# Optimization experiments

Hardware: AMD Instinct MI355X
Metric: run time of the kernel (lower is better)

## Reference

```python
import jax, jax.numpy as jnp
import numpy as np

B, T, N_POS, N_ACT, H = 256, 512, 128, 32, 512
D = N_POS + N_ACT


def setup_inputs() -> dict:
    key = jax.random.key(0)
    ks = jax.random.split(key, 10)
    s_ih = 1.0 / np.sqrt(H)  # torch LSTMCell default uniform(-1/sqrt(H), 1/sqrt(H))
    xav_hc = np.sqrt(2.0 / (B + H))  # xavier_normal_ on [B,H] h0/c0
    return {
        "observation": jax.random.normal(ks[0], (B, T, N_POS), dtype=jnp.float32),
        "action": jax.random.normal(ks[1], (B, T, N_ACT), dtype=jnp.float32),
        "W_ih": jax.random.uniform(ks[2], (4 * H, D), jnp.float32, -s_ih, s_ih),
        "W_hh": jax.random.uniform(ks[3], (4 * H, H), jnp.float32, -s_ih, s_ih),
        "b_ih": jax.random.uniform(ks[4], (4 * H,), jnp.float32, -s_ih, s_ih),
        "b_hh": jax.random.uniform(ks[5], (4 * H,), jnp.float32, -s_ih, s_ih),
        "W_out": jax.random.uniform(ks[6], (1, H), jnp.float32, -s_ih, s_ih),
        "b_out": jax.random.uniform(ks[7], (1,), jnp.float32, -s_ih, s_ih),
        "h0": jax.random.normal(ks[8], (B, H), dtype=jnp.float32) * xav_hc,
        "c0": jax.random.normal(ks[9], (B, H), dtype=jnp.float32) * xav_hc,
    }


def reference(observation, action, W_ih, W_hh, b_ih, b_hh, W_out, b_out, h0, c0):
    # x: [B,T,D] -> scan over time [T,B,D]
    x = jnp.concatenate([observation, action], axis=-1)
    xs = jnp.transpose(x, (1, 0, 2))
    b = b_ih + b_hh

    def step(carry, x_t):
        h, c = carry
        gates = x_t @ W_ih.T + h @ W_hh.T + b  # [B, 4H]
        i, f, g, o = jnp.split(gates, 4, axis=-1)
        i = jax.nn.sigmoid(i)
        f = jax.nn.sigmoid(f)
        g = jnp.tanh(g)
        o = jax.nn.sigmoid(o)
        c_new = f * c + i * g
        h_new = o * jnp.tanh(c_new)
        y = h_new @ W_out.T + b_out  # [B, 1]
        return (h_new, c_new), y

    _, ys = jax.lax.scan(step, (h0, c0), xs)  # ys: [T, B, 1]
    return jnp.transpose(ys, (1, 0, 2))  # [B, T, 1]
```

## Files before the change

kernel.cpp:

```cpp
#include <hip/hip_runtime.h>
#include <math.h>


namespace {
constexpr int kT = 512, kH = 512;

typedef _Float16 v8h __attribute__((ext_vector_type(8)));
typedef float v4f __attribute__((ext_vector_type(4)));
typedef unsigned long long ull;
typedef ull v2u __attribute__((ext_vector_type(2)));

__device__ __forceinline__ ull ld64sc(const ull* p, bool sys) {
    return sys ? __hip_atomic_load(p, __ATOMIC_RELAXED, __HIP_MEMORY_SCOPE_SYSTEM)
               : __hip_atomic_load(p, __ATOMIC_RELAXED, __HIP_MEMORY_SCOPE_AGENT);
}
__device__ __forceinline__ unsigned ld32sc(const unsigned* p, bool sys) {
    return sys ? __hip_atomic_load(p, __ATOMIC_RELAXED, __HIP_MEMORY_SCOPE_SYSTEM)
               : __hip_atomic_load(p, __ATOMIC_RELAXED, __HIP_MEMORY_SCOPE_AGENT);
}
__device__ __forceinline__ void st32sc(unsigned* p, unsigned v, bool sys) {
    if (sys) __hip_atomic_store(p, v, __ATOMIC_RELAXED, __HIP_MEMORY_SCOPE_SYSTEM);
    else     __hip_atomic_store(p, v, __ATOMIC_RELAXED, __HIP_MEMORY_SCOPE_AGENT);
}
__device__ __forceinline__ unsigned ld_sys32(const unsigned* p) {
    return __hip_atomic_load(p, __ATOMIC_RELAXED, __HIP_MEMORY_SCOPE_SYSTEM);
}

__device__ __forceinline__ float sigf(float x) {
    return __builtin_amdgcn_rcpf(1.0f + __expf(fminf(-x, 80.0f)));
}
__device__ __forceinline__ float tanhff(float x) {
    float e = __expf(fminf(2.0f * x, 80.0f));
    return (e - 1.0f) * __builtin_amdgcn_rcpf(e + 1.0f);
}

__global__ void lstm_init(const float* __restrict__ h0, _Float16* __restrict__ hfA,
                          unsigned* __restrict__ ctrl) {
    int i = blockIdx.x * blockDim.x + threadIdx.x;
    int bb = i >> 9, j = i & 511;
    int bgrp = bb >> 4, b = bb & 15;
    int ck = j >> 5, jl = j & 31, qf = jl >> 3, e = jl & 7;
    int slot = (qf * 16 + b) ^ ck;
    hfA[bgrp * 8192 + ck * 512 + slot * 8 + e] = (_Float16)h0[i];
    if (i < 1152) ctrl[i] = 0u;
}

__global__ __launch_bounds__(256, 1) void lstm_persist(
    const float* __restrict__ obs, const float* __restrict__ act,
    const float* __restrict__ Wih, const float* __restrict__ Whh,
    const float* __restrict__ bih, const float* __restrict__ bhh,
    const float* __restrict__ Wout, const float* __restrict__ bout_p,
    const float* __restrict__ c0,
    _Float16* __restrict__ hfA, _Float16* __restrict__ hfB,
    unsigned* __restrict__ ctrl, float* __restrict__ out) {

    __shared__ __align__(16) char actT[26 * 1024];
    __shared__ float ypart[4];
    __shared__ float ytail[2];
    __shared__ int sh_role[3];

    const int tid = threadIdx.x;
    const int w = tid >> 6, ln = tid & 63;
    const int lm = ln & 15, q = ln >> 4;

    unsigned* flags = ctrl;
    unsigned* regcnt = ctrl + 1024;
    unsigned* regtotal = ctrl + 1032;

    if (tid == 0) {
        int x = __builtin_amdgcn_s_getreg(20 | (31 << 11)) & 7;
        unsigned slot = atomicAdd(&regcnt[x], 1u);
        asm volatile("s_waitcnt vmcnt(0)" ::: "memory");
        atomicAdd(regtotal, 1u);
        while (ld_sys32(regtotal) < 256u) __builtin_amdgcn_s_sleep(8);
        unsigned cnt[8];
#pragma unroll
        for (int i = 0; i < 8; ++i) cnt[i] = ld_sys32(&regcnt[i]);
        int pure_base = 0, total_pure = 0, lbase = 0;
        for (int i = 0; i < 8; ++i) {
            if (i < x) { pure_base += cnt[i] >> 4; lbase += cnt[i] & 15; }
            total_pure += cnt[i] >> 4;
        }
        int px16 = (int)(cnt[x] >> 4) * 16;
        int bg, jv, sv;
        if ((int)slot < px16) {
            bg = pure_base + ((int)slot >> 4); jv = slot & 15; sv = 0;
        } else {
            int lr = lbase + ((int)slot - px16);
            bg = total_pure + (lr >> 4); jv = lr & 15; sv = 1;
        }
        sh_role[0] = bg; sh_role[1] = jv; sh_role[2] = sv;
    }
    __syncthreads();
    const int bgrp = sh_role[0], jg = sh_role[1];
    const bool sysS = sh_role[2] != 0;
    const int yb = bgrp * 16 + jg;
    unsigned* myflags = flags + bgrp * 64;

    v8h afrag[2][21];
    {
        const int jj = lm >> 2, gt = lm & 3;
#pragma unroll
        for (int ti = 0; ti < 2; ++ti) {
            const int grow = gt * kH + jg * 32 + w * 8 + jj * 2 + ti;
#pragma unroll
            for (int kc = 0; kc < 21; ++kc) {
                const int k0 = kc * 32 + q * 8;
                const float* src = (k0 < 160) ? (Wih + grow * 160 + k0)
                                              : (Whh + (size_t)grow * kH + (k0 - 160));
                float4 A = *(const float4*)src;
                float4 Bv = *(const float4*)(src + 4);
                v8h f;
                f[0] = (_Float16)A.x;  f[1] = (_Float16)A.y;
                f[2] = (_Float16)A.z;  f[3] = (_Float16)A.w;
                f[4] = (_Float16)Bv.x; f[5] = (_Float16)Bv.y;
                f[6] = (_Float16)Bv.z; f[7] = (_Float16)Bv.w;
                afrag[ti][kc] = f;
            }
        }
    }
    float biasv[2][4];
    float creg[2];
#pragma unroll
    for (int ti = 0; ti < 2; ++ti) {
        const int jloc = jg * 32 + w * 8 + q * 2 + ti;
#pragma unroll
        for (int g = 0; g < 4; ++g)
            biasv[ti][g] = bih[g * kH + jloc] + bhh[g * kH + jloc];
        creg[ti] = c0[(size_t)(bgrp * 16 + lm) * kH + jloc];
    }

    const float bout0 = bout_p[0];
    const float2 wout2 = *(const float2*)(Wout + 2 * tid);
    float4 wout4 = make_float4(0.f, 0.f, 0.f, 0.f);
    if (tid < 128) wout4 = *(const float4*)(Wout + tid * 4);

    const int st = tid - 96, xb = st & 15, c10 = st >> 4;
    const bool isX = (tid >= 96);
    float4 xr[4];

    auto x_load = [&](int tt) {
        if (isX) {
            const size_t brow = (size_t)(bgrp * 16 + xb) * kT + tt;
            const float* p = (c10 < 8) ? (obs + brow * 128 + c10 * 16)
                                       : (act + brow * 32 + (c10 - 8) * 16);
            xr[0] = *(const float4*)(p);
            xr[1] = *(const float4*)(p + 4);
            xr[2] = *(const float4*)(p + 8);
            xr[3] = *(const float4*)(p + 12);
        }
    };
    auto x_write = [&](char* xbase) {
        if (isX) {
            const int kcx = c10 >> 1;
#pragma unroll
            for (int ii = 0; ii < 2; ++ii) {
                const int qx = (2 * c10 + ii) & 3;
                const int slot = (qx * 16 + xb) ^ kcx;
                float4 a = xr[2 * ii], b = xr[2 * ii + 1];
                v8h f;
                f[0] = (_Float16)a.x; f[1] = (_Float16)a.y;
                f[2] = (_Float16)a.z; f[3] = (_Float16)a.w;
                f[4] = (_Float16)b.x; f[5] = (_Float16)b.y;
                f[6] = (_Float16)b.z; f[7] = (_Float16)b.w;
                *(v8h*)(xbase + kcx * 1024 + slot * 16) = f;
            }
        }
    };

    x_load(0);
    x_write(actT);
    __syncthreads();

    char* const hreg = actT + 10240;
    char* const hfAc = (char*)hfA;
    char* const hfBc = (char*)hfB;

#pragma unroll 1
    for (int t = 0; t < kT; ++t) {
        const char* hsrcB = ((t & 1) ? hfBc : hfAc) + (size_t)bgrp * 16384;
        char* hdstB = ((t & 1) ? hfAc : hfBc) + (size_t)bgrp * 16384;
        char* xcur = actT + ((t & 1) ? 5120 : 0);
        char* xnxt = actT + (((t + 1) & 1) ? 5120 : 0);

        if (t < kT - 1) x_load(t + 1);

        if (t > 0 && tid < 64) {
            const unsigned tgt = (unsigned)t;
            const unsigned* fp = myflags + ln;
            while (true) {
                unsigned v = ld32sc(fp, sysS);
                if (__all((int)(v >= tgt))) break;
                __builtin_amdgcn_s_sleep(1);
            }
        }
        __syncthreads();

        if (t >= 2 && tid == 64)
            out[(size_t)yb * kT + (t - 2)] =
                bout0 + ypart[0] + ypart[1] + ypart[2] + ypart[3];

        ull u[8];
#pragma unroll
        for (int k = 0; k < 4; ++k) {
            const ull* sp = (const ull*)(hsrcB + k * 4096 + tid * 16);
            u[2 * k]     = ld64sc(sp, sysS);
            u[2 * k + 1] = ld64sc(sp + 1, sysS);
        }

        v4f a0 = {biasv[0][0], biasv[0][1], biasv[0][2], biasv[0][3]};
        v4f a1 = {biasv[1][0], biasv[1][1], biasv[1][2], biasv[1][3]};
#pragma unroll
        for (int kc = 0; kc < 5; ++kc) {
            v8h bfr = *(const v8h*)(xcur + kc * 1024 + (ln ^ kc) * 16);
            a0 = __builtin_amdgcn_mfma_f32_16x16x32_f16(afrag[0][kc], bfr, a0, 0, 0, 0);
            a1 = __builtin_amdgcn_mfma_f32_16x16x32_f16(afrag[1][kc], bfr, a1, 0, 0, 0);
        }

#pragma unroll
        for (int k = 0; k < 4; ++k) {
            v2u val = {u[2 * k], u[2 * k + 1]};
            *(v2u*)(hreg + k * 4096 + tid * 16) = val;
        }
        x_write(xnxt);
        __syncthreads();

        v4f b0 = {0.f, 0.f, 0.f, 0.f}, b1 = {0.f, 0.f, 0.f, 0.f};
#pragma unroll
        for (int ck = 0; ck < 8; ++ck) {
            v8h bfr = *(const v8h*)(hreg + ck * 1024 + (ln ^ ck) * 16);
            a0 = __builtin_amdgcn_mfma_f32_16x16x32_f16(afrag[0][5 + ck], bfr, a0, 0, 0, 0);
            a1 = __builtin_amdgcn_mfma_f32_16x16x32_f16(afrag[1][5 + ck], bfr, a1, 0, 0, 0);
        }
#pragma unroll
        for (int ck = 8; ck < 16; ++ck) {
            v8h bfr = *(const v8h*)(hreg + ck * 1024 + (ln ^ ck) * 16);
            b0 = __builtin_amdgcn_mfma_f32_16x16x32_f16(afrag[0][5 + ck], bfr, b0, 0, 0, 0);
            b1 = __builtin_amdgcn_mfma_f32_16x16x32_f16(afrag[1][5 + ck], bfr, b1, 0, 0, 0);
        }

        union { unsigned u32; _Float16 h2[2]; } pk;
#pragma unroll
        for (int ti = 0; ti < 2; ++ti) {
            v4f a = ti ? (a1 + b1) : (a0 + b0);
            float iv = sigf(a[0]), fv = sigf(a[1]);
            float gv = tanhff(a[2]), ov = sigf(a[3]);
            creg[ti] = fmaf(fv, creg[ti], iv * gv);
            pk.h2[ti] = (_Float16)(ov * tanhff(creg[ti]));
        }
        st32sc((unsigned*)(hdstB + jg * 1024 + (w * 16 + (lm ^ jg)) * 16 + q * 4),
               pk.u32, sysS);
        asm volatile("s_waitcnt vmcnt(0)" ::: "memory");
        if (ln == 0) st32sc(myflags + jg * 4 + w, (unsigned)(t + 1), sysS);

        if (t > 0) {
            const int k = 2 * tid;
            const int ck = k >> 5, qy = (k >> 3) & 3, e = k & 7;
            const int slot = (qy * 16 + jg) ^ ck;
            union { unsigned uu; _Float16 hh[2]; } cv;
            cv.uu = *(const unsigned*)(hreg + ck * 1024 + slot * 16 + e * 2);
            float p = (float)cv.hh[0] * wout2.x + (float)cv.hh[1] * wout2.y;
#pragma unroll
            for (int s = 32; s; s >>= 1) p += __shfl_xor(p, s);
            if (ln == 0) ypart[w] = p;
        }
    }

    if (tid < 64) {
        const unsigned* fp = myflags + ln;
        while (true) {
            unsigned v = ld32sc(fp, sysS);
            if (__all((int)(v >= (unsigned)kT))) break;
            __builtin_amdgcn_s_sleep(1);
        }
    }
    __syncthreads();
    if (tid == 64)
        out[(size_t)yb * kT + (kT - 2)] =
            bout0 + ypart[0] + ypart[1] + ypart[2] + ypart[3];
    if (tid < 128) {
        const int j0 = tid * 4;
        const int ck = j0 >> 5, qf = (j0 >> 3) & 3, e0 = j0 & 7;
        const int slot = (qf * 16 + jg) ^ ck;
        union { ull uu; _Float16 h4[4]; } cv;
        cv.uu = ld64sc((const ull*)(hfAc + (size_t)bgrp * 16384 + ck * 1024 +
                                    slot * 16 + e0 * 2), sysS);
        float p = (float)cv.h4[0] * wout4.x + (float)cv.h4[1] * wout4.y +
                  (float)cv.h4[2] * wout4.z + (float)cv.h4[3] * wout4.w;
#pragma unroll
        for (int s = 32; s; s >>= 1) p += __shfl_xor(p, s);
        if (ln == 0) ytail[w] = p;
    }
    __syncthreads();
    if (tid == 0) out[(size_t)yb * kT + (kT - 1)] = ytail[0] + ytail[1] + bout0;
}

}

extern "C" void kernel_launch(void* const* d_in, const int* in_sizes, int n_in,
                              void* d_out, int out_size, void* d_ws, size_t ws_size,
                              hipStream_t stream) {
    const float* obs  = (const float*)d_in[0];
    const float* act  = (const float*)d_in[1];
    const float* Wih  = (const float*)d_in[2];
    const float* Whh  = (const float*)d_in[3];
    const float* bih  = (const float*)d_in[4];
    const float* bhh  = (const float*)d_in[5];
    const float* Wout = (const float*)d_in[6];
    const float* bout = (const float*)d_in[7];
    const float* h0   = (const float*)d_in[8];
    const float* c0   = (const float*)d_in[9];
    float* out = (float*)d_out;

    char* ws = (char*)d_ws;
    _Float16* hfA = (_Float16*)ws;
    _Float16* hfB = (_Float16*)(ws + 262144);
    unsigned* ctrl = (unsigned*)(ws + 524288);

    lstm_init<<<512, 256, 0, stream>>>(h0, hfA, ctrl);
    lstm_persist<<<256, 256, 0, stream>>>(obs, act, Wih, Whh, bih, bhh, Wout, bout,
                                          c0, hfA, hfB, ctrl, out);
}
```

Baseline: 1.602 ms.

## Double-buffer h/y shared buffers to drop per-step barrier and cheapen activations

Splits the shared scratch into double-buffered x and h staging areas and a double-buffered ypart array. This lets every wave poll the dependency flags and removes the first __syncthreads per timestep. The x prefetch moves to the end of the step, two steps ahead, so the global load overlaps more of the recurrence. Sigmoid and tanh now use raw exp2 and rcp with no clamping, which cuts instructions on the serial critical path but relies on hardware inf and rcp behaviour at extreme inputs.

```diff
diff --git a/kernel.cpp b/kernel.cpp
--- a/kernel.cpp
+++ b/kernel.cpp
@@ -27,11 +27,12 @@
 }
 
 __device__ __forceinline__ float sigf(float x) {
-    return __builtin_amdgcn_rcpf(1.0f + __expf(fminf(-x, 80.0f)));
+    return __builtin_amdgcn_rcpf(1.0f + __builtin_amdgcn_exp2f(x * -1.442695041f));
 }
 __device__ __forceinline__ float tanhff(float x) {
-    float e = __expf(fminf(2.0f * x, 80.0f));
-    return (e - 1.0f) * __builtin_amdgcn_rcpf(e + 1.0f);
+    return fmaf(-2.0f,
+                __builtin_amdgcn_rcpf(__builtin_amdgcn_exp2f(x * 2.885390082f) + 1.0f),
+                1.0f);
 }
 
 __global__ void lstm_init(const float* __restrict__ h0, _Float16* __restrict__ hfA,
@@ -54,8 +55,9 @@
     _Float16* __restrict__ hfA, _Float16* __restrict__ hfB,
     unsigned* __restrict__ ctrl, float* __restrict__ out) {
 
-    __shared__ __align__(16) char actT[26 * 1024];
-    __shared__ float ypart[4];
+    __shared__ __align__(16) char xbuf[2][5 * 1024];
+    __shared__ __align__(16) char hbuf[2][16 * 1024];
+    __shared__ float ypart[2][4];
     __shared__ float ytail[2];
     __shared__ int sh_role[3];
 
@@ -169,10 +171,10 @@
     };
 
     x_load(0);
-    x_write(actT);
+    x_write(xbuf[0]);
+    x_load(1);
     __syncthreads();
 
-    char* const hreg = actT + 10240;
     char* const hfAc = (char*)hfA;
     char* const hfBc = (char*)hfB;
 
@@ -180,25 +182,17 @@
     for (int t = 0; t < kT; ++t) {
         const char* hsrcB = ((t & 1) ? hfBc : hfAc) + (size_t)bgrp * 16384;
         char* hdstB = ((t & 1) ? hfAc : hfBc) + (size_t)bgrp * 16384;
-        char* xcur = actT + ((t & 1) ? 5120 : 0);
-        char* xnxt = actT + (((t + 1) & 1) ? 5120 : 0);
-
-        if (t < kT - 1) x_load(t + 1);
-
-        if (t > 0 && tid < 64) {
+        const char* xcur = xbuf[t & 1];
+        char* hreg = hbuf[t & 1];
+
+        if (t > 0) {
             const unsigned tgt = (unsigned)t;
             const unsigned* fp = myflags + ln;
             while (true) {
                 unsigned v = ld32sc(fp, sysS);
                 if (__all((int)(v >= tgt))) break;
-                __builtin_amdgcn_s_sleep(1);
             }
         }
-        __syncthreads();
-
-        if (t >= 2 && tid == 64)
-            out[(size_t)yb * kT + (t - 2)] =
-                bout0 + ypart[0] + ypart[1] + ypart[2] + ypart[3];
 
         ull u[8];
 #pragma unroll
@@ -222,8 +216,13 @@
             v2u val = {u[2 * k], u[2 * k + 1]};
             *(v2u*)(hreg + k * 4096 + tid * 16) = val;
         }
-        x_write(xnxt);
+        if (t < kT - 1) x_write(xbuf[(t + 1) & 1]);
         __syncthreads();
+
+        if (t >= 2 && tid == 64) {
+            const float* yp = ypart[(t - 1) & 1];
+            out[(size_t)yb * kT + (t - 2)] = bout0 + yp[0] + yp[1] + yp[2] + yp[3];
+        }
 
         v4f b0 = {0.f, 0.f, 0.f, 0.f}, b1 = {0.f, 0.f, 0.f, 0.f};
 #pragma unroll
@@ -262,8 +261,10 @@
             float p = (float)cv.hh[0] * wout2.x + (float)cv.hh[1] * wout2.y;
 #pragma unroll
             for (int s = 32; s; s >>= 1) p += __shfl_xor(p, s);
-            if (ln == 0) ypart[w] = p;
-        }
+            if (ln == 0) ypart[t & 1][w] = p;
+        }
+
+        if (t < kT - 2) x_load(t + 2);
     }
 
     if (tid < 64) {
@@ -275,9 +276,10 @@
         }
     }
     __syncthreads();
-    if (tid == 64)
-        out[(size_t)yb * kT + (kT - 2)] =
-            bout0 + ypart[0] + ypart[1] + ypart[2] + ypart[3];
+    if (tid == 64) {
+        const float* yp = ypart[1];
+        out[(size_t)yb * kT + (kT - 2)] = bout0 + yp[0] + yp[1] + yp[2] + yp[3];
+    }
     if (tid < 128) {
         const int j0 = tid * 4;
         const int ck = j0 >> 5, qf = (j0 >> 3) & 3, e0 = j0 & 7;
```

Result: slower. 1.769 ms (+10.4%).
